# Kernel optimization log

Measured on AMD Instinct MI355X. Metric: run time of the kernel, lower is better.

## Reference

```python
import jax, jax.numpy as jnp
import numpy as np

EPS = 1e-5
B, C = 8192, 64   # batch == hidden_dim, channels == input_dim (= imf_nums + 1)
CR = C // 4       # rate = 4


def setup_inputs() -> dict:
    key = jax.random.key(0)
    ks = jax.random.split(key, 10)
    g = lambda k, s: jax.random.normal(k, s, dtype=jnp.float32)
    return {
        "pred": g(ks[0], (B, 1)),
        "imfs": g(ks[1], (B, C - 1)),  # columns = the torch list of (B,1) imfs
        "rev_w": jnp.ones((C,), jnp.float32),
        "rev_b": jnp.zeros((C,), jnp.float32),
        "ca_w1": g(ks[2], (CR, C)) * 0.1, "ca_b1": jnp.zeros((CR,), jnp.float32),
        "ca_w2": g(ks[3], (C, CR)) * 0.1, "ca_b2": jnp.zeros((C,), jnp.float32),
        "conv1_w": g(ks[4], (CR, C, 7)) * 0.1, "conv1_b": jnp.zeros((CR,), jnp.float32),
        "bn1_gamma": jnp.ones((CR,), jnp.float32), "bn1_beta": jnp.zeros((CR,), jnp.float32),
        "bn1_mean": g(ks[5], (CR,)) * 0.1,
        "bn1_var": jax.random.uniform(ks[6], (CR,), jnp.float32) + 0.5,
        "conv2_w": g(ks[7], (C, CR, 7)) * 0.1, "conv2_b": jnp.zeros((C,), jnp.float32),
        "bn2_gamma": jnp.ones((C,), jnp.float32), "bn2_beta": jnp.zeros((C,), jnp.float32),
        "bn2_mean": g(ks[8], (C,)) * 0.1,
        "bn2_var": jax.random.uniform(ks[9], (C,), jnp.float32) + 0.5,
    }


def _bn(x, gamma, beta, mean, var):
    # BatchNorm1d in inference mode (running stats), per-channel on last axis
    return (x - mean) * jax.lax.rsqrt(var + EPS) * gamma + beta


def reference(pred, imfs, rev_w, rev_b, ca_w1, ca_b1, ca_w2, ca_b2,
              conv1_w, conv1_b, bn1_gamma, bn1_beta, bn1_mean, bn1_var,
              conv2_w, conv2_b, bn2_gamma, bn2_beta, bn2_mean, bn2_var):
    data = jnp.concatenate([pred, imfs], axis=1)               # (B, C) = cat([pred]+imfs, dim=1)
    # RevIN norm: detached global stats (dim2reduce=() on 2D -> full reduction), affine per feature
    mu = jax.lax.stop_gradient(jnp.mean(data))
    std = jax.lax.stop_gradient(jnp.sqrt(jnp.var(data) + EPS))
    x_norm = (data - mu) / std * rev_w + rev_b                 # (B, C)
    # channel attention: h=w=1 so the Linear MLP acts per-sample on the channel axis
    att = jax.nn.relu(x_norm @ ca_w1.T + ca_b1) @ ca_w2.T + ca_b2
    x = x_norm * att                                           # (B, C)
    # spatial attention: Conv1d(k=7, pad=3) on length-1 sequences == center-tap (index 3) matmul
    h = jax.nn.relu(_bn(x @ conv1_w[:, :, 3].T + conv1_b, bn1_gamma, bn1_beta, bn1_mean, bn1_var))
    h = _bn(h @ conv2_w[:, :, 3].T + conv2_b, bn2_gamma, bn2_beta, bn2_mean, bn2_var)
    out = x * jax.nn.sigmoid(h)                                # (B, C)
    w = out.reshape(B, C)                                      # (hidden_dim, input_dim); B == hidden_dim
    w = (w - rev_b) / (rev_w + EPS * EPS) * std + mu           # RevIN denorm
    # reconstructed = sum_i signal_i (B,1) * w[:, i] (hidden,) -> (B, hidden) broadcast sum == GEMM
    recon = jnp.einsum('bc,hc->bh', data, w)                   # (B, B)
    return recon, w, data, x_norm
```

## Files before the change

### kernel.cpp

```cpp
#include <hip/hip_runtime.h>
#include <hip/hip_bf16.h>

typedef __hip_bfloat16 bf16;
typedef __attribute__((ext_vector_type(8))) short short8;
typedef __attribute__((ext_vector_type(4))) float f32x4;

#define B_    8192
#define C_    64
#define NTOT  524288
#define OUT_W_OFF    67108864
#define OUT_DATA_OFF (OUT_W_OFF + NTOT)
#define OUT_XN_OFF   (OUT_DATA_OFF + NTOT)

__global__ __launch_bounds__(256) void reduce_kernel(const float* __restrict__ pred,
                                                     const float* __restrict__ imfs,
                                                     float* __restrict__ sums) {
    float s = 0.f, s2 = 0.f;
    int tid = blockIdx.x * blockDim.x + threadIdx.x;
    int stride = gridDim.x * blockDim.x;
    const f32x4* p4 = (const f32x4*)pred;
    const f32x4* i4 = (const f32x4*)imfs;
    for (int i = tid; i < B_ / 4; i += stride) {
        f32x4 v = p4[i];
        s += v.x + v.y + v.z + v.w;
        s2 += v.x * v.x + v.y * v.y + v.z * v.z + v.w * v.w;
    }
    for (int i = tid; i < (B_ * (C_ - 1)) / 4; i += stride) {
        f32x4 v = i4[i];
        s += v.x + v.y + v.z + v.w;
        s2 += v.x * v.x + v.y * v.y + v.z * v.z + v.w * v.w;
    }
    #pragma unroll
    for (int off = 32; off > 0; off >>= 1) {
        s  += __shfl_down(s,  off, 64);
        s2 += __shfl_down(s2, off, 64);
    }
    __shared__ float ls[4], ls2[4];
    int wv = threadIdx.x >> 6, ln = threadIdx.x & 63;
    if (ln == 0) { ls[wv] = s; ls2[wv] = s2; }
    __syncthreads();
    if (threadIdx.x == 0) {
        float a = 0.f, b = 0.f;
        for (int i = 0; i < 4; i++) { a += ls[i]; b += ls2[i]; }
        atomicAdd(&sums[0], a);
        atomicAdd(&sums[1], b);
    }
}

__global__ __launch_bounds__(256) void rows_kernel(
    const float* __restrict__ pred, const float* __restrict__ imfs,
    const float* __restrict__ rev_w, const float* __restrict__ rev_b,
    const float* __restrict__ ca_w1, const float* __restrict__ ca_b1,
    const float* __restrict__ ca_w2, const float* __restrict__ ca_b2,
    const float* __restrict__ conv1_w, const float* __restrict__ conv1_b,
    const float* __restrict__ bn1_g, const float* __restrict__ bn1_b,
    const float* __restrict__ bn1_m, const float* __restrict__ bn1_v,
    const float* __restrict__ conv2_w, const float* __restrict__ conv2_b,
    const float* __restrict__ bn2_g, const float* __restrict__ bn2_b,
    const float* __restrict__ bn2_m, const float* __restrict__ bn2_v,
    const float* __restrict__ sums,
    float* __restrict__ out_w, float* __restrict__ out_data,
    float* __restrict__ out_xn,
    bf16* __restrict__ dhi, bf16* __restrict__ whi) {

    __shared__ float w1s[16 * 65];
    __shared__ float w2s[64 * 17];
    __shared__ float c1s[16 * 65];
    __shared__ float c2s[64 * 17];
    __shared__ float xnb[4][64];
    __shared__ float h1b[4][16];

    for (int i = threadIdx.x; i < 1024; i += 256) {
        int j = i >> 6, c = i & 63;
        w1s[j * 65 + c] = ca_w1[i];
        c1s[j * 65 + c] = conv1_w[i * 7 + 3];
    }
    for (int i = threadIdx.x; i < 1024; i += 256) {
        int c = i >> 4, j = i & 15;
        w2s[c * 17 + j] = ca_w2[i];
        c2s[c * 17 + j] = conv2_w[i * 7 + 3];
    }
    __syncthreads();

    const int c   = threadIdx.x & 63;
    const int wv  = threadIdx.x >> 6;
    const int jj  = c & 15;
    const int q16 = (c >> 4) * 16;

    const float revw = rev_w[c], revb = rev_b[c];
    const float cab2 = ca_b2[c], c2b = conv2_b[c];
    const float bn2s = bn2_g[c] * rsqrtf(bn2_v[c] + 1e-5f);
    const float bn2h = bn2_b[c] - bn2_m[c] * bn2s;
    const float cab1 = ca_b1[jj], c1b = conv1_b[jj];
    const float bn1s = bn1_g[jj] * rsqrtf(bn1_v[jj] + 1e-5f);
    const float bn1h = bn1_b[jj] - bn1_m[jj] * bn1s;

    const float inv_n = 1.0f / (float)NTOT;
    const float mu   = sums[0] * inv_n;
    const float var  = sums[1] * inv_n - mu * mu;
    const float stdv = sqrtf(var + 1e-5f);
    const float istd = 1.0f / stdv;

    const int gw = blockIdx.x * 4 + wv;
    for (int row = gw; row < B_; row += 2048) {
        float d = (c == 0) ? pred[row] : imfs[row * 63 + c - 1];
        out_data[row * 64 + c] = d;
        dhi[row * 64 + c] = __float2bfloat16(d);
        float xn = (d - mu) * istd * revw + revb;
        out_xn[row * 64 + c] = xn;
        xnb[wv][c] = xn;
        __builtin_amdgcn_wave_barrier();
        float p1 = 0.f;
        #pragma unroll
        for (int i = 0; i < 16; i++) p1 += w1s[jj * 65 + q16 + i] * xnb[wv][q16 + i];
        p1 += __shfl_xor(p1, 16, 64);
        p1 += __shfl_xor(p1, 32, 64);
        float y = fmaxf(p1 + cab1, 0.f);
        if (c < 16) h1b[wv][c] = y;
        __builtin_amdgcn_wave_barrier();
        float att = cab2;
        #pragma unroll
        for (int j = 0; j < 16; j++) att += w2s[c * 17 + j] * h1b[wv][j];
        float x = xn * att;
        xnb[wv][c] = x;
        __builtin_amdgcn_wave_barrier();
        float p2 = 0.f;
        #pragma unroll
        for (int i = 0; i < 16; i++) p2 += c1s[jj * 65 + q16 + i] * xnb[wv][q16 + i];
        p2 += __shfl_xor(p2, 16, 64);
        p2 += __shfl_xor(p2, 32, 64);
        float t = fmaxf((p2 + c1b) * bn1s + bn1h, 0.f);
        if (c < 16) h1b[wv][c] = t;
        __builtin_amdgcn_wave_barrier();
        float v = c2b;
        #pragma unroll
        for (int j = 0; j < 16; j++) v += c2s[c * 17 + j] * h1b[wv][j];
        v = v * bn2s + bn2h;
        float sg = 1.0f / (1.0f + __expf(-v));
        float ov = x * sg;
        float wval = (ov - revb) / (revw + 1e-10f) * stdv + mu;
        out_w[row * 64 + c] = wval;
        whi[row * 64 + c] = __float2bfloat16(wval);
        __builtin_amdgcn_wave_barrier();
    }
}

__global__ __launch_bounds__(256) void gemm_kernel(
    const bf16* __restrict__ dhi, const bf16* __restrict__ whi,
    float* __restrict__ out) {

    __shared__ float tile[64 * 132];

    const int lane = threadIdx.x & 63;
    const int wv   = threadIdx.x >> 6;
    const int m    = lane & 15;
    const int q    = lane >> 4;
    const int r0b  = blockIdx.y * 64;
    const int rw   = wv * 16;
    const int c0   = blockIdx.x * 128;

    const short* dptr = (const short*)dhi;
    const short* hptr = (const short*)whi;

    short8 a0 = *(const short8*)(dptr + (r0b + rw + m) * 64 + q * 8);
    short8 a1 = *(const short8*)(dptr + (r0b + rw + m) * 64 + q * 8 + 32);

    #pragma unroll
    for (int t = 0; t < 8; t++) {
        const int h = c0 + t * 16 + m;
        short8 b0 = *(const short8*)(hptr + h * 64 + q * 8);
        short8 b1 = *(const short8*)(hptr + h * 64 + q * 8 + 32);
        f32x4 a = {0.f, 0.f, 0.f, 0.f};
        a = __builtin_amdgcn_mfma_f32_16x16x32_bf16(a0, b0, a, 0, 0, 0);
        a = __builtin_amdgcn_mfma_f32_16x16x32_bf16(a1, b1, a, 0, 0, 0);
        #pragma unroll
        for (int r = 0; r < 4; r++)
            tile[(rw + q * 4 + r) * 132 + t * 16 + m] = a[r];
    }
    __syncthreads();

    #pragma unroll
    for (int p = 0; p < 8; p++) {
        const int rl = p * 8 + (threadIdx.x >> 5);
        const int cl = (threadIdx.x & 31) * 4;
        f32x4 v = *(const f32x4*)&tile[rl * 132 + cl];
        *(f32x4*)&out[(long)(r0b + rl) * B_ + c0 + cl] = v;
    }
}

extern "C" void kernel_launch(void* const* d_in, const int* in_sizes, int n_in,
                              void* d_out, int out_size, void* d_ws, size_t ws_size,
                              hipStream_t stream) {
    const float* pred    = (const float*)d_in[0];
    const float* imfs    = (const float*)d_in[1];
    const float* rev_w   = (const float*)d_in[2];
    const float* rev_b   = (const float*)d_in[3];
    const float* ca_w1   = (const float*)d_in[4];
    const float* ca_b1   = (const float*)d_in[5];
    const float* ca_w2   = (const float*)d_in[6];
    const float* ca_b2   = (const float*)d_in[7];
    const float* conv1_w = (const float*)d_in[8];
    const float* conv1_b = (const float*)d_in[9];
    const float* bn1_g   = (const float*)d_in[10];
    const float* bn1_b   = (const float*)d_in[11];
    const float* bn1_m   = (const float*)d_in[12];
    const float* bn1_v   = (const float*)d_in[13];
    const float* conv2_w = (const float*)d_in[14];
    const float* conv2_b = (const float*)d_in[15];
    const float* bn2_g   = (const float*)d_in[16];
    const float* bn2_b   = (const float*)d_in[17];
    const float* bn2_m   = (const float*)d_in[18];
    const float* bn2_v   = (const float*)d_in[19];

    float* out  = (float*)d_out;
    float* sums = (float*)d_ws;
    bf16*  dhi  = (bf16*)((char*)d_ws + 16);
    bf16*  whi  = dhi + NTOT;

    hipMemsetAsync(d_ws, 0, 16, stream);
    reduce_kernel<<<256, 256, 0, stream>>>(pred, imfs, sums);
    rows_kernel<<<512, 256, 0, stream>>>(pred, imfs, rev_w, rev_b, ca_w1, ca_b1,
                                         ca_w2, ca_b2, conv1_w, conv1_b,
                                         bn1_g, bn1_b, bn1_m, bn1_v,
                                         conv2_w, conv2_b, bn2_g, bn2_b, bn2_m, bn2_v,
                                         sums,
                                         out + OUT_W_OFF, out + OUT_DATA_OFF,
                                         out + OUT_XN_OFF, dhi, whi);
    dim3 grid(B_ / 128, B_ / 64);
    gemm_kernel<<<grid, 256, 0, stream>>>(dhi, whi, out);
}
```

Measured before the change: 364.0 us.

## Swap GEMM operands to store MFMA output directly, drop LDS staging

The GEMM kernel now swaps the A/B operands, so each lane's MFMA accumulator holds four consecutive output columns and can be written straight to global memory as a 16-byte nontemporal store. This removes the shared-memory tile, its barrier and the LDS round trip. Each wave now covers 16 rows by 512 columns, and the grid becomes a 1D launch of 2048 blocks with a 4-block occupancy hint. The risk is that each store instruction writes 16 scattered 64-byte row segments rather than fully contiguous rows, which could hurt write coalescing on a kernel bound by its 256 MB output.

```diff
diff --git a/kernel.cpp b/kernel.cpp
--- a/kernel.cpp
+++ b/kernel.cpp
@@ -145,46 +145,35 @@
     }
 }
 
-__global__ __launch_bounds__(256) void gemm_kernel(
+__global__ __launch_bounds__(256, 4) void gemm_kernel(
     const bf16* __restrict__ dhi, const bf16* __restrict__ whi,
     float* __restrict__ out) {
 
-    __shared__ float tile[64 * 132];
-
+    const int wid  = (blockIdx.x << 2) + (threadIdx.x >> 6);
     const int lane = threadIdx.x & 63;
-    const int wv   = threadIdx.x >> 6;
     const int m    = lane & 15;
     const int q    = lane >> 4;
-    const int r0b  = blockIdx.y * 64;
-    const int rw   = wv * 16;
-    const int c0   = blockIdx.x * 128;
+
+    const int b0 = (wid >> 4) * 16;
+    const int h0 = (wid & 15) * 512;
 
     const short* dptr = (const short*)dhi;
-    const short* hptr = (const short*)whi;
-
-    short8 a0 = *(const short8*)(dptr + (r0b + rw + m) * 64 + q * 8);
-    short8 a1 = *(const short8*)(dptr + (r0b + rw + m) * 64 + q * 8 + 32);
-
-    #pragma unroll
-    for (int t = 0; t < 8; t++) {
-        const int h = c0 + t * 16 + m;
-        short8 b0 = *(const short8*)(hptr + h * 64 + q * 8);
-        short8 b1 = *(const short8*)(hptr + h * 64 + q * 8 + 32);
-        f32x4 a = {0.f, 0.f, 0.f, 0.f};
-        a = __builtin_amdgcn_mfma_f32_16x16x32_bf16(a0, b0, a, 0, 0, 0);
-        a = __builtin_amdgcn_mfma_f32_16x16x32_bf16(a1, b1, a, 0, 0, 0);
-        #pragma unroll
-        for (int r = 0; r < 4; r++)
-            tile[(rw + q * 4 + r) * 132 + t * 16 + m] = a[r];
-    }
-    __syncthreads();
-
-    #pragma unroll
-    for (int p = 0; p < 8; p++) {
-        const int rl = p * 8 + (threadIdx.x >> 5);
-        const int cl = (threadIdx.x & 31) * 4;
-        f32x4 v = *(const f32x4*)&tile[rl * 132 + cl];
-        *(f32x4*)&out[(long)(r0b + rl) * B_ + c0 + cl] = v;
+    const short* wptr = (const short*)whi;
+
+    short8 d0 = *(const short8*)(dptr + (b0 + m) * 64 + q * 8);
+    short8 d1 = *(const short8*)(dptr + (b0 + m) * 64 + q * 8 + 32);
+
+    float* orow = out + (long)(b0 + m) * B_ + h0 + q * 4;
+
+    #pragma unroll 4
+    for (int t = 0; t < 32; t++) {
+        const int h = h0 + t * 16 + m;
+        short8 a0 = *(const short8*)(wptr + h * 64 + q * 8);
+        short8 a1 = *(const short8*)(wptr + h * 64 + q * 8 + 32);
+        f32x4 acc = {0.f, 0.f, 0.f, 0.f};
+        acc = __builtin_amdgcn_mfma_f32_16x16x32_bf16(a0, d0, acc, 0, 0, 0);
+        acc = __builtin_amdgcn_mfma_f32_16x16x32_bf16(a1, d1, acc, 0, 0, 0);
+        __builtin_nontemporal_store(acc, (f32x4*)(orow + t * 16));
     }
 }
 
@@ -226,6 +215,5 @@
                                          sums,
                                          out + OUT_W_OFF, out + OUT_DATA_OFF,
                                          out + OUT_XN_OFF, dhi, whi);
-    dim3 grid(B_ / 128, B_ / 64);
-    gemm_kernel<<<grid, 256, 0, stream>>>(dhi, whi, out);
-}
+    gemm_kernel<<<2048, 256, 0, stream>>>(dhi, whi, out);
+}
```

Measured after the change: 358.5 us. Within noise of the previous version (-1.5%).
